# Optimization experiments

Hardware: AMD Instinct MI355X
Metric: run time of the kernel (lower is better)

## Reference

```python
import jax, jax.numpy as jnp
import numpy as np

N, NFEAT, NHID, NHEADS, NCLASS, NLAYERS = 4096, 1024, 256, 4, 1024, 2
LRELU_ALPHA = 0.2
MASK_NEG = -9e15


def setup_inputs() -> dict:
    key = jax.random.key(0)
    ks = jax.random.split(key, 6)
    x = jax.random.normal(ks[0], (N, NFEAT), dtype=jnp.float32)
    # dense 0/1 adjacency with guaranteed self-loops (gen_adj always has diag=1)
    adj = jax.random.randint(ks[1], (N, N), 0, 2, dtype=jnp.int32)
    adj = jnp.maximum(adj, jnp.eye(N, dtype=jnp.int32))
    W_heads = jax.random.normal(ks[2], (NLAYERS, NHEADS, NFEAT, NHID), dtype=jnp.float32) / np.sqrt(NFEAT)
    a_heads = jax.random.normal(ks[3], (NLAYERS, NHEADS, 2 * NHID), dtype=jnp.float32) / np.sqrt(2 * NHID)
    W_out = jax.random.normal(ks[4], (NLAYERS, NHID * NHEADS, NCLASS), dtype=jnp.float32) / np.sqrt(NHID * NHEADS)
    a_out = jax.random.normal(ks[5], (NLAYERS, 2 * NCLASS), dtype=jnp.float32) / np.sqrt(2 * NCLASS)
    return {"x": x, "adj": adj, "W_heads": W_heads, "a_heads": a_heads,
            "W_out": W_out, "a_out": a_out}


def _gat_layer(x, mask, W, a):
    """Single GraphAttentionLayer (pyGAT): masked softmax attention over dense adj."""
    Wh = x @ W                              # [N, d]
    d = W.shape[-1]
    f_src = Wh @ a[:d]                      # [N]
    f_dst = Wh @ a[d:]                      # [N]
    e = jax.nn.leaky_relu(f_src[:, None] + f_dst[None, :], LRELU_ALPHA)  # [N, N]
    att = jax.nn.softmax(jnp.where(mask, e, MASK_NEG), axis=-1)
    return att @ Wh                         # [N, d]


def reference(x, adj, W_heads, a_heads, W_out, a_out):
    mask = adj > 0
    n = x.shape[0]
    for l in range(W_heads.shape[0]):       # ConGAT stack (nlayers, small & fixed)
        x_in = x
        # multi-head attention, concat over heads (each head applies ELU: concat=True)
        heads = jax.vmap(lambda W, a: jax.nn.elu(_gat_layer(x_in, mask, W, a)))(
            W_heads[l], a_heads[l])          # [H, N, nhid]
        h = jnp.transpose(heads, (1, 0, 2)).reshape(n, -1)   # [N, H*nhid]
        out = jax.nn.elu(_gat_layer(h, mask, W_out[l], a_out[l]))  # out_att, concat=False, then F.elu
        x = x_in + out                      # residual in ConGAT.forward
    return x
```

## Files before the change

kernel.cpp:

```cpp
#include <hip/hip_runtime.h>
#include <hip/hip_bf16.h>
#include <stdint.h>

#define NN 4096
#define FF 1024
#define LOG2E 1.44269504088896340736f

typedef unsigned short u16;
typedef float f32x4 __attribute__((ext_vector_type(4)));
typedef __bf16 bf16x8 __attribute__((ext_vector_type(8)));

typedef __attribute__((address_space(1))) void gvoid_t;
typedef __attribute__((address_space(3))) void lvoid_t;

__device__ __forceinline__ u16 f2b(float f) {
  __bf16 b = (__bf16)f;
  return __builtin_bit_cast(u16, b);
}
__device__ __forceinline__ float b2f(u16 u) {
  return (float)__builtin_bit_cast(__bf16, u);
}
__device__ __forceinline__ void gload_lds16(const void* g, void* l) {
  __builtin_amdgcn_global_load_lds((gvoid_t*)g, (lvoid_t*)l, 16, 0, 0);
}

__global__ void k_pack(const int* __restrict__ adj, uint32_t* __restrict__ bits) {
  int gw = (blockIdx.x * 256 + threadIdx.x) >> 6;
  int lane = threadIdx.x & 63;
  int row = gw >> 6;
  int j0 = (gw & 63) << 6;
  int a = adj[(long)row * NN + j0 + lane];
  unsigned long long m = __ballot(a != 0);
  if (lane == 0)
    *reinterpret_cast<unsigned long long*>(&bits[row * 128 + (j0 >> 5)]) = m;
}

__global__ void k_cvt(const float* __restrict__ in, u16* __restrict__ out, int n4) {
  int i = blockIdx.x * 256 + threadIdx.x;
  if (i >= n4) return;
  float4 v = reinterpret_cast<const float4*>(in)[i];
  ushort4 o;
  o.x = f2b(v.x); o.y = f2b(v.y); o.z = f2b(v.z); o.w = f2b(v.w);
  reinterpret_cast<ushort4*>(out)[i] = o;
}

__global__ void k_tconv(const float* __restrict__ in, u16* __restrict__ out, int R, int C) {
  __shared__ float t[32][33];
  long bs = (long)R * C;
  const float* ip = in + blockIdx.z * bs;
  u16* op = out + blockIdx.z * bs;
  int r0 = blockIdx.x * 32, c0 = blockIdx.y * 32;
  int tx = threadIdx.x, ty = threadIdx.y;
#pragma unroll
  for (int k = 0; k < 4; k++)
    t[ty + k * 8][tx] = ip[(long)(r0 + ty + k * 8) * C + c0 + tx];
  __syncthreads();
#pragma unroll
  for (int k = 0; k < 4; k++)
    op[(long)(c0 + ty + k * 8) * R + r0 + tx] = f2b(t[tx][ty + k * 8]);
}

__global__ void k_fsd2(const u16* __restrict__ WhT, const float* __restrict__ a,
                       float* __restrict__ s, float* __restrict__ d, int dh) {
  int i = blockIdx.x * 256 + threadIdx.x;
  int h = blockIdx.z;
  int c0 = blockIdx.y * 32;
  const u16* w = WhT + ((long)h * dh + c0) * NN + i;
  const float* as = a + (long)h * 2 * dh + c0;
  const float* ad = as + dh;
  float ss = 0.f, dd = 0.f;
#pragma unroll
  for (int c = 0; c < 32; c++) {
    float v = b2f(w[(long)c * NN]);
    ss = fmaf(v, as[c], ss);
    dd = fmaf(v, ad[c], dd);
  }
  atomicAdd(&s[h * NN + i], ss * LOG2E);
  atomicAdd(&d[h * NN + i], dd * LOG2E);
}

template <int H>
__global__ void k_maxd(const uint32_t* __restrict__ bits, const float* __restrict__ s,
                       const float* __restrict__ d, float* __restrict__ m) {
  int wv = threadIdx.x >> 6, lane = threadIdx.x & 63;
  int row = blockIdx.x * 4 + wv;
  const uint32_t* br = bits + (long)row * 128;
  float mx[H];
#pragma unroll
  for (int h = 0; h < H; h++) mx[h] = -1e30f;
  for (int t = 0; t < 64; t++) {
    int j = t * 64 + lane;
    uint32_t wb = br[j >> 5];
    bool on = (wb >> (j & 31)) & 1u;
#pragma unroll
    for (int h = 0; h < H; h++) {
      float dv = d[h * NN + j];
      mx[h] = (on && dv > mx[h]) ? dv : mx[h];
    }
  }
#pragma unroll
  for (int h = 0; h < H; h++) {
    float v = mx[h];
#pragma unroll
    for (int o = 32; o >= 1; o >>= 1) v = fmaxf(v, __shfl_xor(v, o));
    if (lane == 0) {
      float e = s[h * NN + row] + v;
      m[h * NN + row] = fmaxf(e, 0.2f * e);
    }
  }
}

__global__ __launch_bounds__(256, 2) void k_gemm(const u16* __restrict__ A,
                                                 const u16* __restrict__ BT,
                                                 u16* __restrict__ CT, int K) {
  __shared__ __align__(16) u16 As[128 * 64];
  __shared__ __align__(16) u16 Bs[128 * 64];
  int tid = threadIdx.x;
  int w = tid >> 6, lane = tid & 63;
  int i0 = blockIdx.x * 128, n0 = blockIdx.y * 128;
  int wr = w >> 1, wc = w & 1;
  int l15 = lane & 15, l4 = lane >> 4;

  f32x4 acc[4][4] = {};

  int srow = lane >> 3;
  int sj = ((lane & 7) ^ srow) * 8;

  for (int kt = 0; kt < K / 64; kt++) {
    int k0 = kt * 64;
    __syncthreads();
#pragma unroll
    for (int t = 0; t < 4; t++) {
      int r = w * 32 + t * 8 + srow;
      gload_lds16(A + (long)(i0 + r) * K + k0 + sj, &As[(w * 32 + t * 8) * 64]);
      gload_lds16(BT + (long)(n0 + r) * K + k0 + sj, &Bs[(w * 32 + t * 8) * 64]);
    }
    __syncthreads();
#pragma unroll
    for (int kc = 0; kc < 2; kc++) {
      bf16x8 af[4], bf[4];
#pragma unroll
      for (int mi = 0; mi < 4; mi++) {
        int r = wr * 64 + mi * 16 + l15;
        int ph = (kc * 4 + l4) ^ (r & 7);
        af[mi] = *reinterpret_cast<const bf16x8*>(&As[r * 64 + ph * 8]);
      }
#pragma unroll
      for (int ni = 0; ni < 4; ni++) {
        int r = wc * 64 + ni * 16 + l15;
        int ph = (kc * 4 + l4) ^ (r & 7);
        bf[ni] = *reinterpret_cast<const bf16x8*>(&Bs[r * 64 + ph * 8]);
      }
#pragma unroll
      for (int mi = 0; mi < 4; mi++)
#pragma unroll
        for (int ni = 0; ni < 4; ni++)
          acc[mi][ni] =
              __builtin_amdgcn_mfma_f32_16x16x32_bf16(af[mi], bf[ni], acc[mi][ni], 0, 0, 0);
    }
  }
#pragma unroll
  for (int mi = 0; mi < 4; mi++) {
    int i = i0 + wr * 64 + mi * 16 + l4 * 4;
#pragma unroll
    for (int ni = 0; ni < 4; ni++) {
      int n = n0 + wc * 64 + ni * 16 + l15;
      ushort4 o;
      o.x = f2b(acc[mi][ni][0]);
      o.y = f2b(acc[mi][ni][1]);
      o.z = f2b(acc[mi][ni][2]);
      o.w = f2b(acc[mi][ni][3]);
      *reinterpret_cast<ushort4*>(&CT[(long)n * NN + i]) = o;
    }
  }
}

template <int MODE>
__global__ __launch_bounds__(256, 2) void k_pv(const uint32_t* __restrict__ bits,
                                               const u16* __restrict__ WT,
                                               const float* __restrict__ sA,
                                               const float* __restrict__ dA,
                                               const float* __restrict__ mA,
                                               u16* __restrict__ hout,
                                               const float* __restrict__ xin,
                                               float* __restrict__ xout,
                                               u16* __restrict__ xbout) {
  __shared__ __align__(16) u16 Bs[2][128 * 64];
  int tid = threadIdx.x;
  int w = tid >> 6, lane = tid & 63;
  int cb = blockIdx.x;
  int i0 = blockIdx.y * 64;
  int h = (MODE == 0) ? (cb >> 1) : 0;

  const u16* Bsrc = WT + (long)cb * 128 * NN;
  const float* dv = dA + (long)h * NN;
  int l15 = lane & 15, l4 = lane >> 4;
  int rbase = i0 + w * 16 + l15;
  float s0 = sA[h * NN + rbase];
  float m0 = mA[h * NN + rbase];
  float Ac = s0 - m0;
  float Bc = 0.2f * s0 - m0;
  const uint8_t* br0 = reinterpret_cast<const uint8_t*>(bits) + (long)rbase * 512;

  f32x4 acc[8] = {};
  float zp0 = 0.f;

  int srow = lane >> 3;
  int sj = ((lane & 7) ^ srow) * 8;

#define STAGE(b, kt_)                                                            \
  {                                                                              \
    int j0_ = (kt_) * 64;                                                        \
    _Pragma("unroll") for (int t = 0; t < 4; t++) {                              \
      int c = w * 32 + t * 8 + srow;                                             \
      gload_lds16(Bsrc + (long)c * NN + j0_ + sj, &Bs[b][c * 64]);               \
    }                                                                            \
  }
#define PREF(kt_)                                                                \
  {                                                                              \
    int jb_ = (kt_) * 64 + l4 * 8;                                               \
    plo[0] = *reinterpret_cast<const f32x4*>(&dv[jb_]);                          \
    phi[0] = *reinterpret_cast<const f32x4*>(&dv[jb_ + 4]);                      \
    plo[1] = *reinterpret_cast<const f32x4*>(&dv[jb_ + 32]);                     \
    phi[1] = *reinterpret_cast<const f32x4*>(&dv[jb_ + 36]);                     \
    pmb[0] = br0[jb_ >> 3];                                                      \
    pmb[1] = br0[(jb_ >> 3) + 4];                                                \
  }

  f32x4 plo[2], phi[2];
  uint32_t pmb[2];
  PREF(0);
  STAGE(0, 0);
  __syncthreads();

  for (int kt = 0; kt < 64; kt++) {
    int cur = kt & 1;
    if (kt < 63) STAGE(cur ^ 1, kt + 1);
    f32x4 clo[2], chi[2];
    uint32_t cmb[2];
#pragma unroll
    for (int kc = 0; kc < 2; kc++) { clo[kc] = plo[kc]; chi[kc] = phi[kc]; cmb[kc] = pmb[kc]; }
    if (kt < 63) PREF(kt + 1);
#pragma unroll
    for (int kc = 0; kc < 2; kc++) {
      uint32_t b0 = cmb[kc];
      bf16x8 a0;
#pragma unroll
      for (int e = 0; e < 8; e++) {
        float dj = (e < 4) ? clo[kc][e] : chi[kc][e - 4];
        float v0 = fmaxf(Ac + dj, fmaf(0.2f, dj, Bc));
        float p0 = ((b0 >> e) & 1u) ? exp2f(v0) : 0.f;
        zp0 += p0;
        a0[e] = (__bf16)p0;
      }
#pragma unroll
      for (int nt = 0; nt < 8; nt++) {
        int c = nt * 16 + l15;
        int ph = (kc * 4 + l4) ^ (c & 7);
        bf16x8 bfr = *reinterpret_cast<const bf16x8*>(&Bs[cur][c * 64 + ph * 8]);
        acc[nt] = __builtin_amdgcn_mfma_f32_16x16x32_bf16(a0, bfr, acc[nt], 0, 0, 0);
      }
    }
    __syncthreads();
  }
#undef STAGE
#undef PREF

  float z0 = zp0;
  z0 += __shfl_xor(z0, 16);
  z0 += __shfl_xor(z0, 32);

  float zr[4];
#pragma unroll
  for (int r = 0; r < 4; r++) zr[r] = __shfl(z0, l4 * 4 + r);
#pragma unroll
  for (int nt = 0; nt < 8; nt++) {
    int col = cb * 128 + nt * 16 + l15;
#pragma unroll
    for (int r = 0; r < 4; r++) {
      int i = i0 + w * 16 + l4 * 4 + r;
      float val = acc[nt][r] / zr[r];
      float o = val > 0.f ? val : exp2f(val * LOG2E) - 1.f;
      long idx = (long)i * FF + col;
      if (MODE == 0) {
        hout[idx] = f2b(o);
      } else {
        float xn = xin[idx] + o;
        xout[idx] = xn;
        xbout[idx] = f2b(xn);
      }
    }
  }
}

extern "C" void kernel_launch(void* const* d_in, const int* in_sizes, int n_in,
                              void* d_out, int out_size, void* d_ws, size_t ws_size,
                              hipStream_t stream) {
  const float* x = (const float*)d_in[0];
  const int* adj = (const int*)d_in[1];
  const float* W_heads = (const float*)d_in[2];
  const float* a_heads = (const float*)d_in[3];
  const float* W_out = (const float*)d_in[4];
  const float* a_out = (const float*)d_in[5];
  float* out = (float*)d_out;

  char* ws = (char*)d_ws;
  uint32_t* bits = (uint32_t*)(ws + 0x0);
  u16* xb = (u16*)(ws + 0x200000);
  u16* WcatT = (u16*)(ws + 0xA00000);
  u16* WoutT = (u16*)(ws + 0xE00000);
  u16* WhT = (u16*)(ws + 0x1200000);
  u16* hbuf = (u16*)(ws + 0x1A00000);
  float* xmid = (float*)(ws + 0x2200000);
  float* s_h = (float*)(ws + 0x3200000);
  float* d_h = (float*)(ws + 0x3210000);
  float* m_h = (float*)(ws + 0x3220000);
  float* s_o = (float*)(ws + 0x3230000);
  float* d_o = (float*)(ws + 0x3234000);
  float* m_o = (float*)(ws + 0x3238000);

  k_pack<<<65536, 256, 0, stream>>>(adj, bits);
  k_cvt<<<4096, 256, 0, stream>>>(x, xb, NN * FF / 4);
  k_tconv<<<dim3(32, 8, 8), dim3(32, 8), 0, stream>>>(W_heads, WcatT, 1024, 256);
  k_tconv<<<dim3(32, 32, 2), dim3(32, 8), 0, stream>>>(W_out, WoutT, 1024, 1024);

  for (int l = 0; l < 2; l++) {
    hipMemsetAsync(ws + 0x3200000, 0, 0x3C000, stream);
    k_gemm<<<dim3(32, 8), 256, 0, stream>>>(xb, WcatT + l * 1048576, WhT, FF);
    k_fsd2<<<dim3(16, 8, 4), 256, 0, stream>>>(WhT, a_heads + l * 2048, s_h, d_h, 256);
    k_maxd<4><<<1024, 256, 0, stream>>>(bits, s_h, d_h, m_h);
    k_pv<0><<<dim3(8, 64), 256, 0, stream>>>(bits, WhT, s_h, d_h, m_h, hbuf, nullptr,
                                             nullptr, nullptr);
    k_gemm<<<dim3(32, 8), 256, 0, stream>>>(hbuf, WoutT + l * 1048576, WhT, FF);
    k_fsd2<<<dim3(16, 32, 1), 256, 0, stream>>>(WhT, a_out + l * 2048, s_o, d_o, 1024);
    k_maxd<1><<<1024, 256, 0, stream>>>(bits, s_o, d_o, m_o);
    k_pv<1><<<dim3(8, 64), 256, 0, stream>>>(bits, WhT, s_o, d_o, m_o, nullptr,
                                             l ? xmid : x, l ? out : xmid, xb);
  }
}
```

Baseline: 660.5 us.

## Materialize attention probabilities in bf16 and run PV as a plain GEMM

Adds a kernel that writes the masked, exponentiated attention matrix P and its row sums Z to workspace in bf16. A separate GEMM kernel then computes P·Wh and applies the normalization, ELU and residual. This replaces the fused k_pv path that regenerated exp values inside the matmul loop, removing transcendental and mask work from the MFMA inner loop. In exchange it writes and reads a large P buffer (about 128 MB for the four heads) through memory, and it only runs when the workspace is big enough.

```diff
diff --git a/kernel.cpp b/kernel.cpp
--- a/kernel.cpp
+++ b/kernel.cpp
@@ -9,6 +9,7 @@
 typedef unsigned short u16;
 typedef float f32x4 __attribute__((ext_vector_type(4)));
 typedef __bf16 bf16x8 __attribute__((ext_vector_type(8)));
+typedef u16 u16x8 __attribute__((ext_vector_type(8)));
 
 typedef __attribute__((address_space(1))) void gvoid_t;
 typedef __attribute__((address_space(3))) void lvoid_t;
@@ -171,6 +172,126 @@
       o.z = f2b(acc[mi][ni][2]);
       o.w = f2b(acc[mi][ni][3]);
       *reinterpret_cast<ushort4*>(&CT[(long)n * NN + i]) = o;
+    }
+  }
+}
+
+__global__ void k_pgen(const uint32_t* __restrict__ bits, const float* __restrict__ sA,
+                       const float* __restrict__ dA, const float* __restrict__ mA,
+                       u16* __restrict__ P, float* __restrict__ Z) {
+  int wv = threadIdx.x >> 6, lane = threadIdx.x & 63;
+  int row = blockIdx.x * 4 + wv;
+  int h = blockIdx.y;
+  const float* dv = dA + (long)h * NN;
+  float s0 = sA[h * NN + row], m0 = mA[h * NN + row];
+  float Ac = s0 - m0;
+  float Bc = 0.2f * s0 - m0;
+  const uint8_t* br = reinterpret_cast<const uint8_t*>(bits) + (long)row * 512;
+  u16* prow = P + (long)h * NN * NN + (long)row * NN;
+  float zp = 0.f;
+#pragma unroll
+  for (int pass = 0; pass < 8; pass++) {
+    int j = pass * 512 + lane * 8;
+    f32x4 dlo = *reinterpret_cast<const f32x4*>(&dv[j]);
+    f32x4 dhi = *reinterpret_cast<const f32x4*>(&dv[j + 4]);
+    uint32_t mb = br[j >> 3];
+    u16x8 o;
+#pragma unroll
+    for (int e = 0; e < 8; e++) {
+      float dj = (e < 4) ? dlo[e] : dhi[e - 4];
+      float v = fmaxf(Ac + dj, fmaf(0.2f, dj, Bc));
+      float p = ((mb >> e) & 1u) ? exp2f(v) : 0.f;
+      zp += p;
+      o[e] = f2b(p);
+    }
+    *reinterpret_cast<u16x8*>(&prow[j]) = o;
+  }
+#pragma unroll
+  for (int off = 32; off >= 1; off >>= 1) zp += __shfl_xor(zp, off);
+  if (lane == 0) Z[h * NN + row] = zp;
+}
+
+template <int MODE>
+__global__ __launch_bounds__(256, 2) void k_pvg(const u16* __restrict__ P,
+                                                const u16* __restrict__ BT,
+                                                const float* __restrict__ Z,
+                                                u16* __restrict__ hout,
+                                                const float* __restrict__ xin,
+                                                float* __restrict__ xout,
+                                                u16* __restrict__ xbout) {
+  __shared__ __align__(16) u16 As[64 * 64];
+  __shared__ __align__(16) u16 Bs[128 * 64];
+  int tid = threadIdx.x;
+  int w = tid >> 6, lane = tid & 63;
+  int i0 = blockIdx.x * 64, n0 = blockIdx.y * 128;
+  int h = (MODE == 0) ? (n0 >> 8) : 0;
+  const u16* A = P + (long)h * NN * NN;
+  const float* Zr = Z + (MODE == 0 ? h * NN : 0);
+  int wr = w >> 1, wc = w & 1;
+  int l15 = lane & 15, l4 = lane >> 4;
+
+  f32x4 acc[2][4] = {};
+
+  int srow = lane >> 3;
+  int sj = ((lane & 7) ^ srow) * 8;
+
+  for (int kt = 0; kt < NN / 64; kt++) {
+    int k0 = kt * 64;
+    __syncthreads();
+#pragma unroll
+    for (int t = 0; t < 2; t++) {
+      int r = w * 16 + t * 8 + srow;
+      gload_lds16(A + (long)(i0 + r) * NN + k0 + sj, &As[(w * 16 + t * 8) * 64]);
+    }
+#pragma unroll
+    for (int t = 0; t < 4; t++) {
+      int r = w * 32 + t * 8 + srow;
+      gload_lds16(BT + (long)(n0 + r) * NN + k0 + sj, &Bs[(w * 32 + t * 8) * 64]);
+    }
+    __syncthreads();
+#pragma unroll
+    for (int kc = 0; kc < 2; kc++) {
+      bf16x8 af[2], bf[4];
+#pragma unroll
+      for (int mi = 0; mi < 2; mi++) {
+        int r = wr * 32 + mi * 16 + l15;
+        int ph = (kc * 4 + l4) ^ (r & 7);
+        af[mi] = *reinterpret_cast<const bf16x8*>(&As[r * 64 + ph * 8]);
+      }
+#pragma unroll
+      for (int ni = 0; ni < 4; ni++) {
+        int r = wc * 64 + ni * 16 + l15;
+        int ph = (kc * 4 + l4) ^ (r & 7);
+        bf[ni] = *reinterpret_cast<const bf16x8*>(&Bs[r * 64 + ph * 8]);
+      }
+#pragma unroll
+      for (int mi = 0; mi < 2; mi++)
+#pragma unroll
+        for (int ni = 0; ni < 4; ni++)
+          acc[mi][ni] =
+              __builtin_amdgcn_mfma_f32_16x16x32_bf16(af[mi], bf[ni], acc[mi][ni], 0, 0, 0);
+    }
+  }
+#pragma unroll
+  for (int mi = 0; mi < 2; mi++) {
+#pragma unroll
+    for (int r = 0; r < 4; r++) {
+      int i = i0 + wr * 32 + mi * 16 + l4 * 4 + r;
+      float zi = Zr[i];
+#pragma unroll
+      for (int ni = 0; ni < 4; ni++) {
+        int col = n0 + wc * 64 + ni * 16 + l15;
+        float val = acc[mi][ni][r] / zi;
+        float o = val > 0.f ? val : exp2f(val * LOG2E) - 1.f;
+        long idx = (long)i * FF + col;
+        if (MODE == 0) {
+          hout[idx] = f2b(o);
+        } else {
+          float xn = xin[idx] + o;
+          xout[idx] = xn;
+          xbout[idx] = f2b(xn);
+        }
+      }
     }
   }
 }
@@ -318,6 +439,10 @@
   float* s_o = (float*)(ws + 0x3230000);
   float* d_o = (float*)(ws + 0x3234000);
   float* m_o = (float*)(ws + 0x3238000);
+  float* Z_h = (float*)(ws + 0x3240000);
+  float* Z_o = (float*)(ws + 0x3250000);
+  u16* Pbuf = (u16*)(ws + 0x3400000);
+  bool bigws = ws_size >= 0xB400000ull;
 
   k_pack<<<65536, 256, 0, stream>>>(adj, bits);
   k_cvt<<<4096, 256, 0, stream>>>(x, xb, NN * FF / 4);
@@ -329,12 +454,24 @@
     k_gemm<<<dim3(32, 8), 256, 0, stream>>>(xb, WcatT + l * 1048576, WhT, FF);
     k_fsd2<<<dim3(16, 8, 4), 256, 0, stream>>>(WhT, a_heads + l * 2048, s_h, d_h, 256);
     k_maxd<4><<<1024, 256, 0, stream>>>(bits, s_h, d_h, m_h);
-    k_pv<0><<<dim3(8, 64), 256, 0, stream>>>(bits, WhT, s_h, d_h, m_h, hbuf, nullptr,
-                                             nullptr, nullptr);
+    if (bigws) {
+      k_pgen<<<dim3(1024, 4), 256, 0, stream>>>(bits, s_h, d_h, m_h, Pbuf, Z_h);
+      k_pvg<0><<<dim3(64, 8), 256, 0, stream>>>(Pbuf, WhT, Z_h, hbuf, nullptr, nullptr,
+                                                nullptr);
+    } else {
+      k_pv<0><<<dim3(8, 64), 256, 0, stream>>>(bits, WhT, s_h, d_h, m_h, hbuf, nullptr,
+                                               nullptr, nullptr);
+    }
     k_gemm<<<dim3(32, 8), 256, 0, stream>>>(hbuf, WoutT + l * 1048576, WhT, FF);
     k_fsd2<<<dim3(16, 32, 1), 256, 0, stream>>>(WhT, a_out + l * 2048, s_o, d_o, 1024);
     k_maxd<1><<<1024, 256, 0, stream>>>(bits, s_o, d_o, m_o);
-    k_pv<1><<<dim3(8, 64), 256, 0, stream>>>(bits, WhT, s_o, d_o, m_o, nullptr,
-                                             l ? xmid : x, l ? out : xmid, xb);
-  }
-}
+    if (bigws) {
+      k_pgen<<<dim3(1024, 1), 256, 0, stream>>>(bits, s_o, d_o, m_o, Pbuf, Z_o);
+      k_pvg<1><<<dim3(64, 8), 256, 0, stream>>>(Pbuf, WhT, Z_o, nullptr, l ? xmid : x,
+                                                l ? out : xmid, xb);
+    } else {
+      k_pv<1><<<dim3(8, 64), 256, 0, stream>>>(bits, WhT, s_o, d_o, m_o, nullptr,
+                                               l ? xmid : x, l ? out : xmid, xb);
+    }
+  }
+}
```

Measured after the change: 574.4 us. -13.0%, faster.
